# Kernel tuning notes

Measured on AMD Instinct MI355X. Metric: run time of the kernel, lower is better.

The kernel has to match this reference:

```python
import jax, jax.numpy as jnp
import numpy as np
from jax import lax

SEQ_LEN, PRED_LEN = 336, 336
T_TOT = SEQ_LEN + PRED_LEN
D_MODEL, D_FF = 128, 256
NUM_KERNELS, TOP_K = 6, 2
PERIOD_COEFF = 0.9
WAVELET_SCALE = 8
N_SCALES = 8
KMAX = 2 * NUM_KERNELS - 1  # 11 (largest Inception kernel)
PREC = 10  # wavelet integration precision (2**PREC samples), as in ptwt/pywt


def _kernel_mask():
    # Inception_Block_V1 kernel i has size (2i+1); embed each centered in a KMAX x KMAX
    # zero kernel -> identical 'same' convolution, lets us fuse all branches into one conv.
    m = np.zeros((NUM_KERNELS, 1, 1, KMAX, KMAX), np.float32)
    c = KMAX // 2
    for i in range(NUM_KERNELS):
        m[i, :, :, c - i:c + i + 1, c - i:c + i + 1] = 1.0
    return jnp.asarray(m)

MASK = _kernel_mask()


def _cwt_filters():
    # pywt/ptwt 'morl': psi(t)=exp(-t^2/2)cos(5t) on [-8,8], int_psi = cumsum(psi)*dt
    x = np.linspace(-8.0, 8.0, 2 ** PREC)
    psi = np.exp(-x ** 2 / 2.0) * np.cos(5.0 * x)
    step = x[1] - x[0]
    int_psi = np.cumsum(psi) * step
    scales = 2.0 ** np.linspace(-1.0, float(WAVELET_SCALE), N_SCALES)
    filters = []
    for s in scales:
        j = (np.arange(s * (x[-1] - x[0]) + 1) / (s * step)).astype(np.int64)
        j = j[j < int_psi.size]
        # pywt uses np.convolve(data, int_psi[j][::-1]); cross-correlating with the
        # UN-reversed filter is the same operation.
        filters.append(jnp.asarray(int_psi[j], jnp.float32))
    return scales, filters

SCALES, FILTERS = _cwt_filters()


def _conv2d(x, w, b, pad, groups=1):
    y = lax.conv_general_dilated(x, w, (1, 1), pad,
                                 dimension_numbers=('NCHW', 'OIHW', 'NCHW'),
                                 feature_group_count=groups)
    return y + b[None, :, None, None]


def _period_conv(x, W1, b1, W2, b2):
    # Inception(d_model->d_ff) -> GELU -> Inception(d_ff->d_model).
    # mean_i conv(x, W_i) = conv(x, mean_i masked(W_i)) by linearity.
    c = KMAX // 2
    w1 = (W1 * MASK).mean(0)
    w2 = (W2 * MASK).mean(0)
    h = _conv2d(x, w1, b1.mean(0), [(c, c), (c, c)])
    h = jax.nn.gelu(h, approximate=False)
    return _conv2d(h, w2, b2.mean(0), [(c, c), (c, c)])


def _cwt(xc):
    # xc: (C, T) -> (N_SCALES, C, T)
    C, T = xc.shape
    xin = xc[:, None, :]
    outs = []
    for s, f in zip(SCALES, FILTERS):
        L = f.shape[0]
        conv = lax.conv_general_dilated(xin, f[None, None, :], (1,), [(L - 1, L - 1)],
                                        dimension_numbers=('NCH', 'OIH', 'NCH'))[:, 0, :]
        coef = (-np.sqrt(s)) * jnp.diff(conv, axis=-1)  # (C, T+L-2)
        d = (coef.shape[-1] - T) / 2.0
        coef = coef[:, int(np.floor(d)): coef.shape[-1] - int(np.ceil(d))]
        outs.append(coef)
    return jnp.stack(outs, 0)


def _topk_periods(x_np):
    # FFT_for_Period: indices are detached in torch -> compute as host constants.
    xf = np.fft.rfft(x_np, axis=1)
    fl = np.abs(xf).mean(0).mean(-1)
    fl[0] = 0.0
    top = np.argsort(-fl, kind='stable')[:TOP_K].astype(np.int64)
    periods = (x_np.shape[1] // top).astype(np.int64)
    return top, periods


def setup_inputs() -> dict:
    key = jax.random.key(0)
    ks = jax.random.split(key, 7)
    B = 8
    x = jax.random.normal(ks[0], (B, T_TOT, D_MODEL), jnp.float32)
    W1 = jax.random.normal(ks[1], (NUM_KERNELS, D_FF, D_MODEL, KMAX, KMAX), jnp.float32) * 0.02
    b1 = jax.random.normal(ks[2], (NUM_KERNELS, D_FF), jnp.float32) * 0.02
    W2 = jax.random.normal(ks[3], (NUM_KERNELS, D_MODEL, D_FF, KMAX, KMAX), jnp.float32) * 0.02
    b2 = jax.random.normal(ks[4], (NUM_KERNELS, D_MODEL), jnp.float32) * 0.02
    Wsc = jax.random.normal(ks[5], (D_MODEL, 1, N_SCALES, 1), jnp.float32) * 0.1  # depthwise (8,1)
    bsc = jax.random.normal(ks[6], (D_MODEL,), jnp.float32) * 0.02
    return {'x': x, 'W1': W1, 'b1': b1, 'W2': W2, 'b2': b2, 'Wsc': Wsc, 'bsc': bsc}


def _forward(x, W1, b1, W2, b2, Wsc, bsc, top_idx, periods):
    B, T, N = x.shape
    xf = jnp.fft.rfft(x, axis=1)
    pw = jnp.abs(xf).mean(-1)[:, top_idx]  # (B, k)
    branches = []
    for p in periods:
        p = int(p)
        length = -(-T // p) * p
        xp = jnp.pad(x, ((0, 0), (0, length - T), (0, 0)))
        o = xp.reshape(B, length // p, p, N).transpose(0, 3, 1, 2)  # (B,N,L/p,p)
        o = _period_conv(o, W1, b1, W2, b2)
        o = o.transpose(0, 2, 3, 1).reshape(B, length, N)[:, :T, :]
        branches.append(o)
    res = jnp.stack(branches, -1)  # (B,T,N,k)
    w = jax.nn.softmax(pw, axis=1)[:, None, None, :]
    period_out = (res * w).sum(-1)
    # wavelet (CWT) branch
    coeffs = _cwt(x.transpose(0, 2, 1).reshape(B * N, T))  # (8, B*N, T)
    coeffs = coeffs.reshape(N_SCALES, B, N, T).transpose(1, 2, 0, 3)  # (B,N,8,T)
    wr = _period_conv(coeffs, W1, b1, W2, b2)
    wr = _conv2d(wr, Wsc, bsc, [(0, 0), (0, 0)], groups=N)  # (B,N,1,T)
    wr = wr[:, :, 0, :].transpose(0, 2, 1)  # (B,T,N)
    pc10 = PERIOD_COEFF ** 10
    return (1.0 - pc10) * wr + pc10 * period_out + x


def reference(x, W1, b1, W2, b2, Wsc, bsc):
    top_idx, periods = _topk_periods(np.asarray(x))
    return _forward(x, W1, b1, W2, b2, Wsc, bsc, jnp.asarray(top_idx), periods)
```

## Files before the change

### kernel.cpp

```cpp
#include <hip/hip_runtime.h>
#include <math.h>
#include <stdint.h>

#define TT 672
#define NFREQ 337
#define DM 128
#define DFF 256
#define QP_CWT 5456
#define QPB 2048
#define BROWS 272
#define ROWSP 9552

typedef float f32x4 __attribute__((ext_vector_type(4)));
typedef short short8 __attribute__((ext_vector_type(8)));

struct FiltParams { int L[8]; int off[8]; int doff[8]; };

__device__ inline unsigned short f2b(float f) {
  unsigned u = __float_as_uint(f);
  return (unsigned short)((u + 0x7FFFu + ((u >> 16) & 1u)) >> 16);
}
__device__ inline float b2f(unsigned short s) {
  return __uint_as_float(((unsigned)s) << 16);
}

__global__ void k_dft(const float* __restrict__ x, float* __restrict__ fl2d) {
  __shared__ float ct[TT], st[TT];
  __shared__ float red[128];
  int f = blockIdx.x, b = blockIdx.y, n = threadIdx.x;
  for (int k = n; k < TT; k += 128) {
    float th = (float)(6.283185307179586 * (double)k / 672.0);
    ct[k] = cosf(th); st[k] = sinf(th);
  }
  __syncthreads();
  float re = 0.f, im = 0.f;
  const float* xb = x + ((size_t)b * TT) * DM + n;
  int k = 0;
  for (int t = 0; t < TT; ++t) {
    float xv = xb[(size_t)t * DM];
    re += xv * ct[k]; im += xv * st[k];
    k += f; if (k >= TT) k -= TT;
  }
  red[n] = sqrtf(re * re + im * im);
  __syncthreads();
  for (int s = 64; s > 0; s >>= 1) { if (n < s) red[n] += red[n + s]; __syncthreads(); }
  if (n == 0) fl2d[b * NFREQ + f] = red[0] * (1.f / 128.f);
}

__global__ void k_ctrl(const float* __restrict__ fl2d,
                       const float* __restrict__ b1, const float* __restrict__ b2,
                       int* __restrict__ ctrl, float* __restrict__ wsm,
                       float* __restrict__ b1e, float* __restrict__ b2e) {
  __shared__ float fl[NFREQ];
  int tid = threadIdx.x;
  for (int f = tid; f < NFREQ; f += 256) {
    float s = 0.f;
    for (int b = 0; b < 8; ++b) s += fl2d[b * NFREQ + f];
    fl[f] = s * 0.125f;
  }
  __syncthreads();
  if (tid == 0) {
    fl[0] = 0.f;
    int t1 = 1; float v1 = fl[1];
    for (int f = 2; f < NFREQ; ++f) if (fl[f] > v1) { v1 = fl[f]; t1 = f; }
    int t2 = (t1 == 1) ? 2 : 1; float v2 = fl[t2];
    for (int f = t2 + 1; f < NFREQ; ++f) { if (f == t1) continue; if (fl[f] > v2) { v2 = fl[f]; t2 = f; } }
    int tops[2] = { t1, t2 };
    for (int kk = 0; kk < 2; ++kk) {
      int p = TT / tops[kk];
      int H = (TT + p - 1) / p;
      int PW = p - 1 < 5 ? p - 1 : 5;
      ctrl[kk * 3 + 0] = p; ctrl[kk * 3 + 1] = PW; ctrl[kk * 3 + 2] = H * (p + 2 * PW);
    }
    ctrl[6] = 672; ctrl[7] = 8; ctrl[8] = QP_CWT;
    for (int b = 0; b < 8; ++b) {
      float p0 = fl2d[b * NFREQ + t1], p1 = fl2d[b * NFREQ + t2];
      float m = fmaxf(p0, p1);
      float e0 = expf(p0 - m), e1 = expf(p1 - m);
      float inv = 1.f / (e0 + e1);
      wsm[b * 2 + 0] = e0 * inv; wsm[b * 2 + 1] = e1 * inv;
    }
  }
  if (tid < 256) { float s = 0.f; for (int i = 0; i < 6; ++i) s += b1[i * DFF + tid]; b1e[tid] = s * (1.f / 6.f); }
  if (tid < 128) { float s = 0.f; for (int i = 0; i < 6; ++i) s += b2[i * DM + tid]; b2e[tid] = s * (1.f / 6.f); }
}

__global__ void k_wprep(const float* __restrict__ W, unsigned short* __restrict__ wl,
                        int Cout, int Cin) {
  int co = blockIdx.x, ci = blockIdx.y, t = threadIdx.x;
  if (t >= 121) return;
  int u = t / 11, v = t - u * 11;
  int du = u - 5; if (du < 0) du = -du;
  int dv = v - 5; if (dv < 0) dv = -dv;
  int m = du > dv ? du : dv;
  size_t kstride = (size_t)Cout * Cin * 121;
  size_t base = ((size_t)co * Cin + ci) * 121 + t;
  float s = 0.f;
  for (int i = m; i < 6; ++i) s += W[i * kstride + base];
  int cot = co >> 7, row = co & 127;
  int c64 = ci >> 6, part = (ci >> 3) & 7, within = ci & 7;
  int nc = Cin >> 6;
  size_t slab = ((size_t)t * (Cout >> 7) + cot) * nc + c64;
  wl[slab * 8192 + row * 64 + (((part ^ (row & 7)) << 3) + within)] = f2b(s * (1.f / 6.f));
}

__global__ void k_filt(float* __restrict__ d, FiltParams fp) {
  __shared__ double ps[1024];
  __shared__ float ip[1024];
  int si = blockIdx.x, tid = threadIdx.x;
  for (int i = tid; i < 1024; i += 256) {
    double xv = -8.0 + (double)i * (16.0 / 1023.0);
    ps[i] = exp(-xv * xv * 0.5) * cos(5.0 * xv);
  }
  __syncthreads();
  if (tid == 0) {
    double acc = 0.0;
    for (int i = 0; i < 1024; ++i) { acc += ps[i]; ip[i] = (float)(acc * (16.0 / 1023.0)); }
  }
  __syncthreads();
  double texp = (si == 7) ? 8.0 : (-1.0 + (double)si * (9.0 / 7.0));
  double s = pow(2.0, texp);
  double sstep = s * (16.0 / 1023.0);
  double sq = sqrt(s);
  int L = fp.L[si];
  float* dd = d + fp.doff[si];
  for (int k = tid; k <= L; k += 256) {
    float fk = 0.f, fkm = 0.f;
    if (k < L) { int j = (int)((double)k / sstep); if (j > 1023) j = 1023; fk = ip[j]; }
    if (k > 0) { int j = (int)((double)(k - 1) / sstep); if (j > 1023) j = 1023; fkm = ip[j]; }
    dd[k] = (float)(-sq * (double)(fkm - fk));
  }
}

__global__ __launch_bounds__(256) void k_cwt(const float* __restrict__ x, const float* __restrict__ d,
                      unsigned short* __restrict__ coef, FiltParams fp) {
  __shared__ float dl[4130];
  int tile = blockIdx.x, si = blockIdx.y, b = blockIdx.z;
  int tid = threadIdx.x;
  int n = tid & 127, g = tid >> 7;
  int L = fp.L[si], off = fp.off[si];
  for (int i = tid; i < L + 33; i += 256) {
    int k = i - 16;
    dl[i] = ((unsigned)k <= (unsigned)L) ? d[fp.doff[si] + k] : 0.f;
  }
  __syncthreads();
  int ta = tile * 16 + g * 8;
  float acc[8];
  #pragma unroll
  for (int j = 0; j < 8; ++j) acc[j] = 0.f;
  int rlo = ta + off - L + 1; if (rlo < 0) rlo = 0;
  int rhi = ta + off + 9; if (rhi > TT) rhi = TT;
  const float* xb = x + ((size_t)b * TT) * DM + n;
  for (int r = rlo; r < rhi; ++r) {
    float xv = xb[(size_t)r * DM];
    int kb16 = 16 + r - ta - off + L - 1;
    #pragma unroll
    for (int j = 0; j < 8; ++j) acc[j] += dl[kb16 - j] * xv;
  }
  unsigned short* op = coef + ((size_t)b * QP_CWT + (size_t)si * 682 + 5 + ta) * DM + n;
  #pragma unroll
  for (int j = 0; j < 8; ++j) op[(size_t)j * DM] = f2b(acc[j]);
}

__global__ void k_cwtpad(unsigned short* __restrict__ coef) {
  int b = blockIdx.x, si = blockIdx.y, n = threadIdx.x;
  for (int r = 0; r < 10; ++r) {
    int q = si * 682 + (r < 5 ? r : 672 + r);
    coef[((size_t)b * QP_CWT + q) * DM + n] = 0;
  }
}

__global__ void k_xpad(const float* __restrict__ x, const int* __restrict__ ctrl,
                       unsigned short* __restrict__ xb0, unsigned short* __restrict__ xb1) {
  int q = blockIdx.x, b = blockIdx.y, n = threadIdx.x;
  for (int slot = 0; slot < 2; ++slot) {
    int p = ctrl[slot * 3], PW = ctrl[slot * 3 + 1], QP = ctrl[slot * 3 + 2];
    if (q >= QP) continue;
    int ppad = p + 2 * PW;
    int row = q / ppad, w = q - row * ppad;
    float val = 0.f;
    if (w >= PW && w < p + PW) {
      int t = row * p + (w - PW);
      if (t < TT) val = x[((size_t)b * TT + t) * DM + n];
    }
    unsigned short* dst = slot == 0 ? xb0 : xb1;
    dst[((size_t)b * QPB + q) * DM + n] = f2b(val);
  }
}

__global__ __launch_bounds__(256, 2) void k_convm(
    const unsigned short* __restrict__ inC, const unsigned short* __restrict__ in0,
    const unsigned short* __restrict__ in1, const unsigned short* __restrict__ wl,
    const float* __restrict__ bias,
    unsigned short* __restrict__ outC, unsigned short* __restrict__ out0,
    unsigned short* __restrict__ out1, unsigned short* __restrict__ partial,
    const int* __restrict__ ctrl, int Cin, int Cout,
    int QSC, int QSB, int doGelu, int mode)
{
  __shared__ __align__(16) unsigned short Blds[BROWS * 64];

  int bid = blockIdx.x;
  int b = bid & 7;
  int r = bid >> 3;
  int job, zz, tile;
  if (r < 44) { job = 2; zz = r / 22; tile = r - zz * 22; }
  else if (r < 58) { int rr = r - 44; job = 0; zz = rr / 7; tile = rr - zz * 7; }
  else { int rr = r - 58; job = 1; zz = rr / 7; tile = rr - zz * 7; }

  int p, QP, PW;
  if (job == 2) { p = 672; PW = 5; QP = QP_CWT; }
  else { p = ctrl[job * 3]; PW = ctrl[job * 3 + 1]; QP = ctrl[job * 3 + 2]; }
  int ppad = p + 2 * PW;
  int q0 = tile * 256;
  if (q0 >= QP) return;

  const unsigned short* in = job == 2 ? inC : (job == 0 ? in0 : in1);
  int QS = job == 2 ? QSC : QSB;
  int jobbase = job == 2 ? 0 : (job == 0 ? QP_CWT : QP_CWT + QPB);

  int nc = Cin >> 6, ncot = Cout >> 7;
  int cotblk, c64lo, c64n;
  if (mode == 0) { cotblk = zz; c64lo = 0; c64n = nc; }
  else { cotblk = 0; c64lo = zz * 2; c64n = 2; }

  int tid = threadIdx.x;
  int wv = tid >> 6, lane = tid & 63;
  int wcx = wv & 1, wqy = wv >> 1;
  int lrow = lane & 15, lhi = lane >> 4;
  int nv = 2 * PW;
  size_t vstride = (size_t)ncot * nc * 16384;

  int aoff0 = (wcx * 64 + lrow) * 128 + ((lhi ^ (lrow & 7)) << 4);
  int aoff1 = (wcx * 64 + lrow) * 128 + (((4 + lhi) ^ (lrow & 7)) << 4);

  f32x4 acc[4][8];
  #pragma unroll
  for (int i = 0; i < 4; ++i)
    #pragma unroll
    for (int j = 0; j < 8; ++j)
      #pragma unroll
      for (int rr = 0; rr < 4; ++rr) acc[i][j][rr] = 0.f;

  const unsigned short* inb = in + (size_t)b * QS * Cin;

  for (int cc = 0; cc < c64n; ++cc) {
    int c64 = c64lo + cc;
    for (int u = 0; u < 11; ++u) {
      int qb0 = q0 - PW + (u - 5) * ppad;
      if (qb0 >= QP || qb0 + 256 + 2 * PW <= 0) continue;
      __syncthreads();
      #pragma unroll
      for (int it = 0; it < 9; ++it) {
        int idx = it * 256 + tid;
        if (idx < BROWS * 8) {
          int row = idx >> 3, part = idx & 7;
          int qs = qb0 + row;
          short8 vv = {0, 0, 0, 0, 0, 0, 0, 0};
          if ((unsigned)qs < (unsigned)QP)
            vv = *(const short8*)&inb[(size_t)qs * Cin + c64 * 64 + part * 8];
          *(short8*)&Blds[row * 64 + ((part ^ (row & 7)) << 3)] = vv;
        }
      }
      __syncthreads();
      size_t slab0b = ((size_t)((u * 11 + 5 - PW) * ncot + cotblk) * nc + c64) * 16384;
      const char* aglb = (const char*)wl + slab0b;
      for (int vi = 0; vi <= nv; ++vi) {
        short8 a0[4], a1[4];
        #pragma unroll
        for (int mi = 0; mi < 4; ++mi)
          a0[mi] = *(const short8*)(aglb + aoff0 + mi * 2048);
        #pragma unroll
        for (int mi = 0; mi < 4; ++mi)
          a1[mi] = *(const short8*)(aglb + aoff1 + mi * 2048);
        __builtin_amdgcn_s_setprio(1);
        {
          short8 bf[8];
          #pragma unroll
          for (int ni = 0; ni < 8; ++ni) {
            int row = wqy * 128 + ni * 16 + lrow + vi;
            bf[ni] = *(const short8*)&Blds[row * 64 + ((lhi ^ (row & 7)) << 3)];
          }
          #pragma unroll
          for (int mi = 0; mi < 4; ++mi)
            #pragma unroll
            for (int ni = 0; ni < 8; ++ni)
              acc[mi][ni] = __builtin_amdgcn_mfma_f32_16x16x32_bf16(a0[mi], bf[ni], acc[mi][ni], 0, 0, 0);
        }
        {
          short8 bf[8];
          #pragma unroll
          for (int ni = 0; ni < 8; ++ni) {
            int row = wqy * 128 + ni * 16 + lrow + vi;
            bf[ni] = *(const short8*)&Blds[row * 64 + (((4 + lhi) ^ (row & 7)) << 3)];
          }
          #pragma unroll
          for (int mi = 0; mi < 4; ++mi)
            #pragma unroll
            for (int ni = 0; ni < 8; ++ni)
              acc[mi][ni] = __builtin_amdgcn_mfma_f32_16x16x32_bf16(a1[mi], bf[ni], acc[mi][ni], 0, 0, 0);
        }
        __builtin_amdgcn_s_setprio(0);
        aglb += vstride;
      }
    }
  }

  if (mode == 0) {
    unsigned short* outp = job == 2 ? outC : (job == 0 ? out0 : out1);
    int qv[8]; bool pad[8];
    #pragma unroll
    for (int ni = 0; ni < 8; ++ni) {
      int q = q0 + wqy * 128 + ni * 16 + lrow;
      qv[ni] = q;
      int w = q - (q / ppad) * ppad;
      pad[ni] = (w < PW) || (w >= p + PW);
    }
    #pragma unroll
    for (int mi = 0; mi < 4; ++mi) {
      int co = cotblk * 128 + wcx * 64 + mi * 16 + lhi * 4;
      float bv0 = bias[co], bv1 = bias[co + 1], bv2 = bias[co + 2], bv3 = bias[co + 3];
      #pragma unroll
      for (int ni = 0; ni < 8; ++ni) {
        int q = qv[ni];
        if (q >= QP) continue;
        float v0 = acc[mi][ni][0] + bv0;
        float v1 = acc[mi][ni][1] + bv1;
        float v2 = acc[mi][ni][2] + bv2;
        float v3 = acc[mi][ni][3] + bv3;
        if (doGelu) {
          v0 = 0.5f * v0 * (1.f + erff(v0 * 0.7071067811865476f));
          v1 = 0.5f * v1 * (1.f + erff(v1 * 0.7071067811865476f));
          v2 = 0.5f * v2 * (1.f + erff(v2 * 0.7071067811865476f));
          v3 = 0.5f * v3 * (1.f + erff(v3 * 0.7071067811865476f));
        }
        if (pad[ni]) { v0 = 0.f; v1 = 0.f; v2 = 0.f; v3 = 0.f; }
        uint2 pk;
        pk.x = (unsigned)f2b(v0) | ((unsigned)f2b(v1) << 16);
        pk.y = (unsigned)f2b(v2) | ((unsigned)f2b(v3) << 16);
        *(uint2*)&outp[((size_t)b * QS + q) * Cout + co] = pk;
      }
    }
  } else {
    unsigned short* pp = partial + (size_t)zz * 8 * ROWSP * 128;
    #pragma unroll
    for (int mi = 0; mi < 4; ++mi) {
      int co = wcx * 64 + mi * 16 + lhi * 4;
      #pragma unroll
      for (int ni = 0; ni < 8; ++ni) {
        int q = q0 + wqy * 128 + ni * 16 + lrow;
        if (q >= QP) continue;
        uint2 pk;
        pk.x = (unsigned)f2b(acc[mi][ni][0]) | ((unsigned)f2b(acc[mi][ni][1]) << 16);
        pk.y = (unsigned)f2b(acc[mi][ni][2]) | ((unsigned)f2b(acc[mi][ni][3]) << 16);
        *(uint2*)&pp[((size_t)b * ROWSP + jobbase + q) * 128 + co] = pk;
      }
    }
  }
}

__global__ void k_combine(const float* __restrict__ x, const unsigned short* __restrict__ P,
    const float* __restrict__ b2e,
    const float* __restrict__ Wsc, const float* __restrict__ bsc,
    const float* __restrict__ wsm, const int* __restrict__ ctrl, float* __restrict__ out) {
  int t = blockIdx.x, b = blockIdx.y, n = threadIdx.x;
  const size_t SL = (size_t)8 * ROWSP * 128;
  const unsigned short* P0 = P;
  const unsigned short* P1 = P + SL;
  float bv = b2e[n];
  float accv = bsc[n];
  #pragma unroll
  for (int s = 0; s < 8; ++s) {
    size_t r = ((size_t)b * ROWSP + (size_t)s * 682 + 5 + t) * 128 + n;
    float wr = b2f(P0[r]) + b2f(P1[r]) + bv;
    accv += wr * Wsc[n * 8 + s];
  }
  int p0 = ctrl[0], PW0 = ctrl[1], p1 = ctrl[3], PW1 = ctrl[4];
  int q0 = (t / p0) * (p0 + 2 * PW0) + PW0 + (t % p0);
  int q1 = (t / p1) * (p1 + 2 * PW1) + PW1 + (t % p1);
  size_t r0 = ((size_t)b * ROWSP + QP_CWT + q0) * 128 + n;
  size_t r1 = ((size_t)b * ROWSP + QP_CWT + QPB + q1) * 128 + n;
  float bo0v = b2f(P0[r0]) + b2f(P1[r0]) + bv;
  float bo1v = b2f(P0[r1]) + b2f(P1[r1]) + bv;
  float po = wsm[b * 2 + 0] * bo0v + wsm[b * 2 + 1] * bo1v;
  size_t xi = ((size_t)b * TT + t) * DM + n;
  out[xi] = 0.6513215599f * accv + 0.3486784401f * po + x[xi];
}

extern "C" void kernel_launch(void* const* d_in, const int* in_sizes, int n_in,
                              void* d_out, int out_size, void* d_ws, size_t ws_size,
                              hipStream_t stream) {
  const float* x   = (const float*)d_in[0];
  const float* W1  = (const float*)d_in[1];
  const float* b1  = (const float*)d_in[2];
  const float* W2  = (const float*)d_in[3];
  const float* b2  = (const float*)d_in[4];
  const float* Wsc = (const float*)d_in[5];
  const float* bsc = (const float*)d_in[6];
  float* out = (float*)d_out;

  char* base = (char*)d_ws;
  size_t off = 0;
  auto alloc = [&](size_t bytes) -> void* {
    void* pp = base + off; off = (off + bytes + 255) & ~(size_t)255; return pp;
  };
  int*   ctrl = (int*)  alloc(32 * 4);
  float* wsm  = (float*)alloc(16 * 4);
  float* b1e  = (float*)alloc(256 * 4);
  float* b2e  = (float*)alloc(128 * 4);
  float* fl2d = (float*)alloc((size_t)8 * NFREQ * 4);
  float* filt = (float*)alloc(8192 * 4);
  unsigned short* wl1  = (unsigned short*)alloc((size_t)121 * 2 * 2 * 8192 * 2);
  unsigned short* wl2  = (unsigned short*)alloc((size_t)121 * 1 * 4 * 8192 * 2);
  unsigned short* coefp= (unsigned short*)alloc((size_t)8 * QP_CWT * DM * 2);
  unsigned short* h1p  = (unsigned short*)alloc((size_t)8 * QP_CWT * DFF * 2);
  unsigned short* h1b0 = (unsigned short*)alloc((size_t)8 * QPB * DFF * 2);
  unsigned short* h1b1 = (unsigned short*)alloc((size_t)8 * QPB * DFF * 2);
  unsigned short* xb0  = (unsigned short*)alloc((size_t)8 * QPB * DM * 2);
  unsigned short* xb1  = (unsigned short*)alloc((size_t)8 * QPB * DM * 2);
  unsigned short* P    = (unsigned short*)alloc((size_t)2 * 8 * ROWSP * 128 * 2);

  FiltParams fp;
  {
    double step = 16.0 / 1023.0;
    int doff = 0;
    for (int i = 0; i < 8; ++i) {
      double t = (i == 7) ? 8.0 : (-1.0 + (double)i * (9.0 / 7.0));
      double s = pow(2.0, t);
      double stop = s * 16.0 + 1.0;
      int nmax = (int)ceil(stop);
      double sstep = s * step;
      int L = 0;
      for (int k = 0; k < nmax; ++k) {
        long j = (long)((double)k / sstep);
        if (j < 1024) L++; else break;
      }
      fp.L[i] = L;
      fp.off[i] = (L - 2) / 2;
      fp.doff[i] = doff;
      doff += L + 1;
    }
  }

  k_dft<<<dim3(NFREQ, 8), 128, 0, stream>>>(x, fl2d);
  k_ctrl<<<1, 256, 0, stream>>>(fl2d, b1, b2, ctrl, wsm, b1e, b2e);
  k_wprep<<<dim3(256, 128), 128, 0, stream>>>(W1, wl1, 256, 128);
  k_wprep<<<dim3(128, 256), 128, 0, stream>>>(W2, wl2, 128, 256);
  k_filt<<<8, 256, 0, stream>>>(filt, fp);
  k_cwt<<<dim3(42, 8, 8), 256, 0, stream>>>(x, filt, coefp, fp);
  k_cwtpad<<<dim3(8, 8), 128, 0, stream>>>(coefp);
  k_xpad<<<dim3(QPB, 8), 128, 0, stream>>>(x, ctrl, xb0, xb1);

  k_convm<<<576, 256, 0, stream>>>(coefp, xb0, xb1, wl1, b1e,
      h1p, h1b0, h1b1, (unsigned short*)nullptr, ctrl, 128, 256, QP_CWT, QPB, 1, 0);
  k_convm<<<576, 256, 0, stream>>>(h1p, h1b0, h1b1, wl2, b2e,
      (unsigned short*)nullptr, (unsigned short*)nullptr, (unsigned short*)nullptr, P,
      ctrl, 256, 128, QP_CWT, QPB, 0, 1);

  k_combine<<<dim3(TT, 8), 128, 0, stream>>>(x, P, b2e, Wsc, bsc, wsm, ctrl, out);
}
```

Baseline: 858.0 us.

## Double-buffer conv input tiles via async global-to-LDS loads with zero guard bands

The conv kernel's input staging changes from register-mediated loads with bounds checks into a single LDS buffer to direct global_load_lds transfers into two LDS buffers. The next tile is prefetched while MFMAs run on the current one. To drop the per-row bounds checks, the activation buffers get zeroed guard rows before and after each batch, cleared with hipMemsetAsync, and the separate CWT pad kernel is removed. The cost is six extra memsets per call, which write more bytes than before, plus twice the LDS footprint, which may limit occupancy.

```diff
diff --git a/kernel.cpp b/kernel.cpp
--- a/kernel.cpp
+++ b/kernel.cpp
@@ -8,7 +8,10 @@
 #define DFF 256
 #define QP_CWT 5456
 #define QPB 2048
-#define BROWS 272
+#define GRD 288
+#define QSC_ALL 6032
+#define QSB_ALL 2624
+#define BROWS 288
 #define ROWSP 9552
 
 typedef float f32x4 __attribute__((ext_vector_type(4)));
@@ -22,6 +25,12 @@
 }
 __device__ inline float b2f(unsigned short s) {
   return __uint_as_float(((unsigned)s) << 16);
+}
+
+__device__ inline void gld16(const void* g, void* l) {
+  __builtin_amdgcn_global_load_lds(
+      (const __attribute__((address_space(1))) unsigned int*)g,
+      (__attribute__((address_space(3))) unsigned int*)l, 16, 0, 0);
 }
 
 __global__ void k_dft(const float* __restrict__ x, float* __restrict__ fl2d) {
@@ -157,17 +166,9 @@
     #pragma unroll
     for (int j = 0; j < 8; ++j) acc[j] += dl[kb16 - j] * xv;
   }
-  unsigned short* op = coef + ((size_t)b * QP_CWT + (size_t)si * 682 + 5 + ta) * DM + n;
+  unsigned short* op = coef + ((size_t)b * QSC_ALL + (size_t)si * 682 + 5 + ta) * DM + n;
   #pragma unroll
   for (int j = 0; j < 8; ++j) op[(size_t)j * DM] = f2b(acc[j]);
-}
-
-__global__ void k_cwtpad(unsigned short* __restrict__ coef) {
-  int b = blockIdx.x, si = blockIdx.y, n = threadIdx.x;
-  for (int r = 0; r < 10; ++r) {
-    int q = si * 682 + (r < 5 ? r : 672 + r);
-    coef[((size_t)b * QP_CWT + q) * DM + n] = 0;
-  }
 }
 
 __global__ void k_xpad(const float* __restrict__ x, const int* __restrict__ ctrl,
@@ -184,7 +185,7 @@
       if (t < TT) val = x[((size_t)b * TT + t) * DM + n];
     }
     unsigned short* dst = slot == 0 ? xb0 : xb1;
-    dst[((size_t)b * QPB + q) * DM + n] = f2b(val);
+    dst[((size_t)b * QSB_ALL + q) * DM + n] = f2b(val);
   }
 }
 
@@ -197,7 +198,7 @@
     const int* __restrict__ ctrl, int Cin, int Cout,
     int QSC, int QSB, int doGelu, int mode)
 {
-  __shared__ __align__(16) unsigned short Blds[BROWS * 64];
+  __shared__ __align__(16) unsigned short Blds[2][BROWS * 64];
 
   int bid = blockIdx.x;
   int b = bid & 7;
@@ -219,9 +220,9 @@
   int jobbase = job == 2 ? 0 : (job == 0 ? QP_CWT : QP_CWT + QPB);
 
   int nc = Cin >> 6, ncot = Cout >> 7;
-  int cotblk, c64lo, c64n;
-  if (mode == 0) { cotblk = zz; c64lo = 0; c64n = nc; }
-  else { cotblk = 0; c64lo = zz * 2; c64n = 2; }
+  int cotblk, c64lo, ncc;
+  if (mode == 0) { cotblk = zz; c64lo = 0; ncc = nc; }
+  else { cotblk = 0; c64lo = zz * 2; ncc = 2; }
 
   int tid = threadIdx.x;
   int wv = tid >> 6, lane = tid & 63;
@@ -229,9 +230,14 @@
   int lrow = lane & 15, lhi = lane >> 4;
   int nv = 2 * PW;
   size_t vstride = (size_t)ncot * nc * 16384;
+  int CinB = Cin * 2;
 
   int aoff0 = (wcx * 64 + lrow) * 128 + ((lhi ^ (lrow & 7)) << 4);
   int aoff1 = (wcx * 64 + lrow) * 128 + (((4 + lhi) ^ (lrow & 7)) << 4);
+
+  int rsub = lane >> 3;
+  int psrc = (lane & 7) ^ (rsub & 7);
+  const char* inG = (const char*)(in + (size_t)b * QS * Cin);
 
   f32x4 acc[4][8];
   #pragma unroll
@@ -241,68 +247,76 @@
       #pragma unroll
       for (int rr = 0; rr < 4; ++rr) acc[i][j][rr] = 0.f;
 
-  const unsigned short* inb = in + (size_t)b * QS * Cin;
-
-  for (int cc = 0; cc < c64n; ++cc) {
-    int c64 = c64lo + cc;
-    for (int u = 0; u < 11; ++u) {
-      int qb0 = q0 - PW + (u - 5) * ppad;
-      if (qb0 >= QP || qb0 + 256 + 2 * PW <= 0) continue;
-      __syncthreads();
-      #pragma unroll
-      for (int it = 0; it < 9; ++it) {
-        int idx = it * 256 + tid;
-        if (idx < BROWS * 8) {
-          int row = idx >> 3, part = idx & 7;
-          int qs = qb0 + row;
-          short8 vv = {0, 0, 0, 0, 0, 0, 0, 0};
-          if ((unsigned)qs < (unsigned)QP)
-            vv = *(const short8*)&inb[(size_t)qs * Cin + c64 * 64 + part * 8];
-          *(short8*)&Blds[row * 64 + ((part ^ (row & 7)) << 3)] = vv;
+  int kkN = ncc * 11;
+  int kk = 0, qb0c = 0, c64c = 0, uc = 0;
+  auto valid = [&](int k, int& qb0o, int& c64o, int& uo) -> bool {
+    int ccl = k / 11; int ul = k - ccl * 11;
+    qb0o = q0 - PW + (ul - 5) * ppad;
+    c64o = c64lo + ccl; uo = ul;
+    return !(qb0o >= QP || qb0o + 256 + 2 * PW <= 0);
+  };
+  while (kk < kkN && !valid(kk, qb0c, c64c, uc)) ++kk;
+  int cur = 0;
+  if (kk < kkN) {
+    const char* src = inG + (ptrdiff_t)(qb0c + wv * 72 + rsub) * CinB + c64c * 128 + psrc * 16;
+    unsigned short* ldsb = &Blds[0][(wv * 72) * 64];
+    #pragma unroll
+    for (int i = 0; i < 9; ++i)
+      gld16(src + (ptrdiff_t)i * 8 * CinB, (char*)ldsb + i * 1024);
+  }
+  while (kk < kkN) {
+    int kn = kk + 1, qb0n = 0, c64n_ = 0, un = 0;
+    while (kn < kkN && !valid(kn, qb0n, c64n_, un)) ++kn;
+    __syncthreads();
+    if (kn < kkN) {
+      const char* src = inG + (ptrdiff_t)(qb0n + wv * 72 + rsub) * CinB + c64n_ * 128 + psrc * 16;
+      unsigned short* ldsb = &Blds[cur ^ 1][(wv * 72) * 64];
+      #pragma unroll
+      for (int i = 0; i < 9; ++i)
+        gld16(src + (ptrdiff_t)i * 8 * CinB, (char*)ldsb + i * 1024);
+    }
+    const unsigned short* Bcur = &Blds[cur][0];
+    size_t slab0b = ((size_t)((uc * 11 + 5 - PW) * ncot + cotblk) * nc + c64c) * 16384;
+    const char* aglb = (const char*)wl + slab0b;
+    for (int vi = 0; vi <= nv; ++vi) {
+      short8 a0[4], a1[4];
+      #pragma unroll
+      for (int mi = 0; mi < 4; ++mi)
+        a0[mi] = *(const short8*)(aglb + aoff0 + mi * 2048);
+      #pragma unroll
+      for (int mi = 0; mi < 4; ++mi)
+        a1[mi] = *(const short8*)(aglb + aoff1 + mi * 2048);
+      __builtin_amdgcn_s_setprio(1);
+      {
+        short8 bf[8];
+        #pragma unroll
+        for (int ni = 0; ni < 8; ++ni) {
+          int row = wqy * 128 + ni * 16 + lrow + vi;
+          bf[ni] = *(const short8*)&Bcur[row * 64 + ((lhi ^ (row & 7)) << 3)];
         }
-      }
-      __syncthreads();
-      size_t slab0b = ((size_t)((u * 11 + 5 - PW) * ncot + cotblk) * nc + c64) * 16384;
-      const char* aglb = (const char*)wl + slab0b;
-      for (int vi = 0; vi <= nv; ++vi) {
-        short8 a0[4], a1[4];
         #pragma unroll
         for (int mi = 0; mi < 4; ++mi)
-          a0[mi] = *(const short8*)(aglb + aoff0 + mi * 2048);
+          #pragma unroll
+          for (int ni = 0; ni < 8; ++ni)
+            acc[mi][ni] = __builtin_amdgcn_mfma_f32_16x16x32_bf16(a0[mi], bf[ni], acc[mi][ni], 0, 0, 0);
+      }
+      {
+        short8 bf[8];
+        #pragma unroll
+        for (int ni = 0; ni < 8; ++ni) {
+          int row = wqy * 128 + ni * 16 + lrow + vi;
+          bf[ni] = *(const short8*)&Bcur[row * 64 + (((4 + lhi) ^ (row & 7)) << 3)];
+        }
         #pragma unroll
         for (int mi = 0; mi < 4; ++mi)
-          a1[mi] = *(const short8*)(aglb + aoff1 + mi * 2048);
-        __builtin_amdgcn_s_setprio(1);
-        {
-          short8 bf[8];
           #pragma unroll
-          for (int ni = 0; ni < 8; ++ni) {
-            int row = wqy * 128 + ni * 16 + lrow + vi;
-            bf[ni] = *(const short8*)&Blds[row * 64 + ((lhi ^ (row & 7)) << 3)];
-          }
-          #pragma unroll
-          for (int mi = 0; mi < 4; ++mi)
-            #pragma unroll
-            for (int ni = 0; ni < 8; ++ni)
-              acc[mi][ni] = __builtin_amdgcn_mfma_f32_16x16x32_bf16(a0[mi], bf[ni], acc[mi][ni], 0, 0, 0);
-        }
-        {
-          short8 bf[8];
-          #pragma unroll
-          for (int ni = 0; ni < 8; ++ni) {
-            int row = wqy * 128 + ni * 16 + lrow + vi;
-            bf[ni] = *(const short8*)&Blds[row * 64 + (((4 + lhi) ^ (row & 7)) << 3)];
-          }
-          #pragma unroll
-          for (int mi = 0; mi < 4; ++mi)
-            #pragma unroll
-            for (int ni = 0; ni < 8; ++ni)
-              acc[mi][ni] = __builtin_amdgcn_mfma_f32_16x16x32_bf16(a1[mi], bf[ni], acc[mi][ni], 0, 0, 0);
-        }
-        __builtin_amdgcn_s_setprio(0);
-        aglb += vstride;
+          for (int ni = 0; ni < 8; ++ni)
+            acc[mi][ni] = __builtin_amdgcn_mfma_f32_16x16x32_bf16(a1[mi], bf[ni], acc[mi][ni], 0, 0, 0);
       }
-    }
+      __builtin_amdgcn_s_setprio(0);
+      aglb += vstride;
+    }
+    cur ^= 1; kk = kn; qb0c = qb0n; c64c = c64n_; uc = un;
   }
 
   if (mode == 0) {
@@ -411,13 +425,20 @@
   float* filt = (float*)alloc(8192 * 4);
   unsigned short* wl1  = (unsigned short*)alloc((size_t)121 * 2 * 2 * 8192 * 2);
   unsigned short* wl2  = (unsigned short*)alloc((size_t)121 * 1 * 4 * 8192 * 2);
-  unsigned short* coefp= (unsigned short*)alloc((size_t)8 * QP_CWT * DM * 2);
-  unsigned short* h1p  = (unsigned short*)alloc((size_t)8 * QP_CWT * DFF * 2);
-  unsigned short* h1b0 = (unsigned short*)alloc((size_t)8 * QPB * DFF * 2);
-  unsigned short* h1b1 = (unsigned short*)alloc((size_t)8 * QPB * DFF * 2);
-  unsigned short* xb0  = (unsigned short*)alloc((size_t)8 * QPB * DM * 2);
-  unsigned short* xb1  = (unsigned short*)alloc((size_t)8 * QPB * DM * 2);
+  unsigned short* coefA= (unsigned short*)alloc((size_t)8 * QSC_ALL * DM * 2);
+  unsigned short* h1pA = (unsigned short*)alloc((size_t)8 * QSC_ALL * DFF * 2);
+  unsigned short* h1b0A= (unsigned short*)alloc((size_t)8 * QSB_ALL * DFF * 2);
+  unsigned short* h1b1A= (unsigned short*)alloc((size_t)8 * QSB_ALL * DFF * 2);
+  unsigned short* xb0A = (unsigned short*)alloc((size_t)8 * QSB_ALL * DM * 2);
+  unsigned short* xb1A = (unsigned short*)alloc((size_t)8 * QSB_ALL * DM * 2);
   unsigned short* P    = (unsigned short*)alloc((size_t)2 * 8 * ROWSP * 128 * 2);
+
+  unsigned short* coefp = coefA + (size_t)GRD * DM;
+  unsigned short* h1p   = h1pA  + (size_t)GRD * DFF;
+  unsigned short* h1b0  = h1b0A + (size_t)GRD * DFF;
+  unsigned short* h1b1  = h1b1A + (size_t)GRD * DFF;
+  unsigned short* xb0   = xb0A  + (size_t)GRD * DM;
+  unsigned short* xb1   = xb1A  + (size_t)GRD * DM;
 
   FiltParams fp;
   {
@@ -441,20 +462,26 @@
     }
   }
 
+  hipMemsetAsync(coefA, 0, (size_t)8 * QSC_ALL * DM * 2, stream);
+  hipMemsetAsync(h1pA,  0, (size_t)8 * QSC_ALL * DFF * 2, stream);
+  hipMemsetAsync(h1b0A, 0, (size_t)8 * QSB_ALL * DFF * 2, stream);
+  hipMemsetAsync(h1b1A, 0, (size_t)8 * QSB_ALL * DFF * 2, stream);
+  hipMemsetAsync(xb0A,  0, (size_t)8 * QSB_ALL * DM * 2, stream);
+  hipMemsetAsync(xb1A,  0, (size_t)8 * QSB_ALL * DM * 2, stream);
+
   k_dft<<<dim3(NFREQ, 8), 128, 0, stream>>>(x, fl2d);
   k_ctrl<<<1, 256, 0, stream>>>(fl2d, b1, b2, ctrl, wsm, b1e, b2e);
   k_wprep<<<dim3(256, 128), 128, 0, stream>>>(W1, wl1, 256, 128);
   k_wprep<<<dim3(128, 256), 128, 0, stream>>>(W2, wl2, 128, 256);
   k_filt<<<8, 256, 0, stream>>>(filt, fp);
   k_cwt<<<dim3(42, 8, 8), 256, 0, stream>>>(x, filt, coefp, fp);
-  k_cwtpad<<<dim3(8, 8), 128, 0, stream>>>(coefp);
   k_xpad<<<dim3(QPB, 8), 128, 0, stream>>>(x, ctrl, xb0, xb1);
 
   k_convm<<<576, 256, 0, stream>>>(coefp, xb0, xb1, wl1, b1e,
-      h1p, h1b0, h1b1, (unsigned short*)nullptr, ctrl, 128, 256, QP_CWT, QPB, 1, 0);
+      h1p, h1b0, h1b1, (unsigned short*)nullptr, ctrl, 128, 256, QSC_ALL, QSB_ALL, 1, 0);
   k_convm<<<576, 256, 0, stream>>>(h1p, h1b0, h1b1, wl2, b2e,
       (unsigned short*)nullptr, (unsigned short*)nullptr, (unsigned short*)nullptr, P,
-      ctrl, 256, 128, QP_CWT, QPB, 0, 1);
+      ctrl, 256, 128, QSC_ALL, QSB_ALL, 0, 1);
 
   k_combine<<<dim3(TT, 8), 128, 0, stream>>>(x, P, b2e, Wsc, bsc, wsm, ctrl, out);
 }
```

Measured after the change: 884.0 us. 3.0% more time.

## Register-tile CWT convolution with rotating filter window and fold pad kernel

Applied to the files above, without the earlier changes.

The CWT kernel now has each thread compute 16 outputs using a rotating 16-entry register window of filter taps read directly from a zero-padded global filter buffer. This replaces the shared-memory filter staging, its barrier, and the two 8-output thread groups, and it reuses each loaded x value across 16 accumulators. The zeroing of the coefficient padding rows moves into the first and last tiles, which removes one kernel launch. In exchange, filter reads become per-thread global (cached) loads, blocks are half the size, and register pressure is higher.

```diff
diff --git a/kernel.cpp b/kernel.cpp
--- a/kernel.cpp
+++ b/kernel.cpp
@@ -10,6 +10,7 @@
 #define QPB 2048
 #define BROWS 272
 #define ROWSP 9552
+#define FPAD 32
 
 typedef float f32x4 __attribute__((ext_vector_type(4)));
 typedef short short8 __attribute__((ext_vector_type(8)));
@@ -124,49 +125,57 @@
   double sq = sqrt(s);
   int L = fp.L[si];
   float* dd = d + fp.doff[si];
+  for (int k = tid; k < FPAD; k += 256) { dd[k] = 0.f; dd[FPAD + L + 1 + k] = 0.f; }
   for (int k = tid; k <= L; k += 256) {
     float fk = 0.f, fkm = 0.f;
     if (k < L) { int j = (int)((double)k / sstep); if (j > 1023) j = 1023; fk = ip[j]; }
     if (k > 0) { int j = (int)((double)(k - 1) / sstep); if (j > 1023) j = 1023; fkm = ip[j]; }
-    dd[k] = (float)(-sq * (double)(fkm - fk));
-  }
-}
-
-__global__ __launch_bounds__(256) void k_cwt(const float* __restrict__ x, const float* __restrict__ d,
+    dd[FPAD + k] = (float)(-sq * (double)(fkm - fk));
+  }
+}
+
+__global__ __launch_bounds__(128) void k_cwt(const float* __restrict__ x, const float* __restrict__ d,
                       unsigned short* __restrict__ coef, FiltParams fp) {
-  __shared__ float dl[4130];
   int tile = blockIdx.x, si = blockIdx.y, b = blockIdx.z;
-  int tid = threadIdx.x;
-  int n = tid & 127, g = tid >> 7;
+  int n = threadIdx.x;
   int L = fp.L[si], off = fp.off[si];
-  for (int i = tid; i < L + 33; i += 256) {
-    int k = i - 16;
-    dl[i] = ((unsigned)k <= (unsigned)L) ? d[fp.doff[si] + k] : 0.f;
-  }
-  __syncthreads();
-  int ta = tile * 16 + g * 8;
-  float acc[8];
+  const float* dp = d + fp.doff[si] + FPAD;
+  int ta = tile * 16;
+  float acc[16];
   #pragma unroll
-  for (int j = 0; j < 8; ++j) acc[j] = 0.f;
+  for (int j = 0; j < 16; ++j) acc[j] = 0.f;
   int rlo = ta + off - L + 1; if (rlo < 0) rlo = 0;
-  int rhi = ta + off + 9; if (rhi > TT) rhi = TT;
-  const float* xb = x + ((size_t)b * TT) * DM + n;
-  for (int r = rlo; r < rhi; ++r) {
-    float xv = xb[(size_t)r * DM];
-    int kb16 = 16 + r - ta - off + L - 1;
-    #pragma unroll
-    for (int j = 0; j < 8; ++j) acc[j] += dl[kb16 - j] * xv;
+  int rhi = ta + off + 17; if (rhi > TT) rhi = TT;
+  int nt = rhi - rlo;
+  int nt16 = (nt + 15) & ~15;
+  int base0 = rlo - ta - off + L - 1;
+  float w[16];
+  #pragma unroll
+  for (int i = 1; i < 16; ++i) w[i] = dp[base0 + i - 16];
+  w[0] = 0.f;
+  const float* xr = x + ((size_t)b * TT + rlo) * DM + n;
+  for (int t = 0; t < nt16; t += 16) {
+    #pragma unroll
+    for (int tt = 0; tt < 16; ++tt) {
+      int r = rlo + t + tt;
+      w[tt] = dp[base0 + t + tt];
+      float xv = (r < TT) ? xr[(size_t)(t + tt) * DM] : 0.f;
+      #pragma unroll
+      for (int j = 0; j < 16; ++j)
+        acc[j] += w[(tt - j) & 15] * xv;
+    }
   }
   unsigned short* op = coef + ((size_t)b * QP_CWT + (size_t)si * 682 + 5 + ta) * DM + n;
   #pragma unroll
-  for (int j = 0; j < 8; ++j) op[(size_t)j * DM] = f2b(acc[j]);
-}
-
-__global__ void k_cwtpad(unsigned short* __restrict__ coef) {
-  int b = blockIdx.x, si = blockIdx.y, n = threadIdx.x;
-  for (int r = 0; r < 10; ++r) {
-    int q = si * 682 + (r < 5 ? r : 672 + r);
-    coef[((size_t)b * QP_CWT + q) * DM + n] = 0;
+  for (int j = 0; j < 16; ++j) op[(size_t)j * DM] = f2b(acc[j]);
+  if (tile == 0) {
+    unsigned short* pz = coef + ((size_t)b * QP_CWT + (size_t)si * 682) * DM + n;
+    #pragma unroll
+    for (int rr = 0; rr < 5; ++rr) pz[(size_t)rr * DM] = 0;
+  } else if (tile == 41) {
+    unsigned short* pz = coef + ((size_t)b * QP_CWT + (size_t)si * 682 + 677) * DM + n;
+    #pragma unroll
+    for (int rr = 0; rr < 5; ++rr) pz[(size_t)rr * DM] = 0;
   }
 }
 
@@ -437,7 +446,7 @@
       fp.L[i] = L;
       fp.off[i] = (L - 2) / 2;
       fp.doff[i] = doff;
-      doff += L + 1;
+      doff += L + 1 + 2 * FPAD;
     }
   }
 
@@ -446,8 +455,7 @@
   k_wprep<<<dim3(256, 128), 128, 0, stream>>>(W1, wl1, 256, 128);
   k_wprep<<<dim3(128, 256), 128, 0, stream>>>(W2, wl2, 128, 256);
   k_filt<<<8, 256, 0, stream>>>(filt, fp);
-  k_cwt<<<dim3(42, 8, 8), 256, 0, stream>>>(x, filt, coefp, fp);
-  k_cwtpad<<<dim3(8, 8), 128, 0, stream>>>(coefp);
+  k_cwt<<<dim3(42, 8, 8), 128, 0, stream>>>(x, filt, coefp, fp);
   k_xpad<<<dim3(QPB, 8), 128, 0, stream>>>(x, ctrl, xb0, xb1);
 
   k_convm<<<576, 256, 0, stream>>>(coefp, xb0, xb1, wl1, b1e,
```

Measured after the change: 776.6 us (median of 2 runs). 1.1x faster.
